# Optimization experiments

Hardware: AMD Instinct MI355X
Metric: run time of the kernel (lower is better)

Reference implementation:

```python
import jax, jax.numpy as jnp
import numpy as np
from jax import lax

B, C_IN, N, K = 4, 128, 4096, 16
C_OUT = 256
EPS = 1e-5


def setup_inputs() -> dict:
    key = jax.random.key(0)
    k1, k2, k3, k4, k5 = jax.random.split(key, 5)
    x = jax.random.normal(k1, (B, C_IN, N, 1), dtype=jnp.float32)
    y = jax.random.normal(k2, (B, C_IN, N, 1), dtype=jnp.float32)
    edge_index = jax.random.randint(k3, (2, B, N, K), 0, N)
    # Conv2d(in=2*C_IN, out=C_OUT, kernel 3x3), kaiming-ish scale
    fan_in = 2 * C_IN * 9
    conv_w = jax.random.normal(k4, (C_OUT, 2 * C_IN, 3, 3), dtype=jnp.float32) * (2.0 / fan_in) ** 0.5
    conv_b = jnp.zeros((C_OUT,), dtype=jnp.float32)
    gamma = jnp.ones((C_OUT,), dtype=jnp.float32)
    beta = jnp.zeros((C_OUT,), dtype=jnp.float32)
    _ = k5
    return {"x": x, "y": y, "edge_index": edge_index,
            "conv_w": conv_w, "conv_b": conv_b, "gamma": gamma, "beta": beta}


def _batched_index_select(feat, idx):
    # feat: [B, C, N, 1], idx: [B, N, K] -> [B, C, N, K]
    fs = feat[..., 0]  # [B, C, N]
    return jax.vmap(lambda fb, ib: fb[:, ib])(fs, idx)


def reference(x, y, edge_index, conv_w, conv_b, gamma, beta):
    x_i = _batched_index_select(x, edge_index[1])        # [B, C, N, K]
    x_j = _batched_index_select(y, edge_index[0])        # [B, C, N, K]
    h = jnp.concatenate([x_i, x_j - x_i], axis=1)        # [B, 2C, N, K]
    out = lax.conv_general_dilated(
        h, conv_w, window_strides=(1, 1), padding=((1, 1), (1, 1)),
        dimension_numbers=("NCHW", "OIHW", "NCHW"))
    out = out + conv_b[None, :, None, None]
    # BatchNorm2d in training mode: biased batch statistics per channel
    mean = jnp.mean(out, axis=(0, 2, 3), keepdims=True)
    var = jnp.mean((out - mean) ** 2, axis=(0, 2, 3), keepdims=True)
    out = gamma[None, :, None, None] * (out - mean) * lax.rsqrt(var + EPS) + beta[None, :, None, None]
    out = jax.nn.relu(out)
    return jnp.max(out, axis=-1, keepdims=True)          # [B, C_OUT, N, 1]
```

## Files before the change

kernel.cpp:

```cpp
#include <hip/hip_runtime.h>

typedef unsigned short u16;
typedef unsigned int u32;
typedef __attribute__((ext_vector_type(8))) u16 u16x8;
typedef __attribute__((ext_vector_type(8))) __bf16 bf16x8;
typedef __attribute__((ext_vector_type(4))) float f32x4;

#define CIN 128
#define NB 4
#define NN 4096
#define KPTS 16
#define COUT 256
#define POSB 65536
#define TOTPOS 262144
#define CK 2304

__device__ __forceinline__ float bf2f(u16 u){ return __uint_as_float(((u32)u)<<16); }
__device__ __forceinline__ u16 f2bf(float f){
  u32 u = __float_as_uint(f);
  u32 r = (u + 0x7fffu + ((u>>16)&1u)) >> 16;
  return (u16)r;
}

__global__ void pack_w_kernel(const float* __restrict__ w, u16* __restrict__ wp){
  int t = blockIdx.x*256 + threadIdx.x;
  if (t >= COUT*CK) return;
  int co = t / CK; int r = t - co*CK; int tap = r >> 8; int c = r & 255;
  float v;
  if (c < 128)
    v = w[(co*256 + c)*9 + tap] - w[(co*256 + 128 + c)*9 + tap];
  else
    v = w[(co*256 + c)*9 + tap];
  wp[t] = f2bf(v);
}

__global__ void transpose_cast_kernel(const float* __restrict__ x, const float* __restrict__ y,
                                      u16* __restrict__ xt, u16* __restrict__ yt){
  __shared__ u16 tile[2][32][65];
  int n0 = blockIdx.x*64, c0 = blockIdx.y*32, b = blockIdx.z;
  int t = threadIdx.x;
  int tn = t & 63, tc = t >> 6;
  #pragma unroll
  for (int i=0;i<8;++i){
    int c = tc*8 + i;
    size_t src = ((size_t)(b*CIN + c0 + c))*NN + n0 + tn;
    tile[0][c][tn] = f2bf(x[src]);
    tile[1][c][tn] = f2bf(y[src]);
  }
  __syncthreads();
  int tcc = t & 31, tnn = t >> 5;
  #pragma unroll
  for (int i=0;i<8;++i){
    int n = tnn*8 + i;
    size_t dst = ((size_t)(b*NN + n0 + n))*CIN + c0 + tcc;
    xt[dst] = tile[0][tcc][n];
    yt[dst] = tile[1][tcc][n];
  }
}

#define SWZ(row, chunk) (((row)*32) + ((((chunk) ^ (((row)>>1)&3))) << 3))

__global__ __launch_bounds__(256) void conv_gemm_kernel(const u16* __restrict__ wp,
    const int* __restrict__ e, const u16* __restrict__ xt, const u16* __restrict__ yt,
    const u16* __restrict__ zrow, const float* __restrict__ bias,
    float* __restrict__ ssum, float* __restrict__ ssq, float* __restrict__ maxout){
  __shared__ u16 als[3*4096];
  __shared__ u16 pnl[2*6144];

  int bid = blockIdx.x;
  int co_half = (bid >> 3) & 1;
  int ptile = (bid & 7) | ((bid >> 4) << 3);
  int p0 = ptile * 128;
  int b = p0 >> 16;
  int pib0 = p0 & (POSB-1);
  int nb0 = pib0 >> 4;

  int t = threadIdx.x;
  int lane = t & 63, wave = t >> 6;
  int wr = wave >> 1, wc = wave & 1;
  int co_base = co_half*128;
  int l15 = lane & 15, l4 = lane >> 4;

  const u16* xb = xt + ((size_t)b)*NN*CIN;
  const u16* yb = yt + ((size_t)b)*NN*CIN;

  int r0 = wave*32 + (lane>>2);
  int r1 = r0 + 16;
  int ch0 = (lane&3) ^ ((r0>>1)&3);
  int ch1 = (lane&3) ^ ((r1>>1)&3);
  int wuni = __builtin_amdgcn_readfirstlane(wave);
  int wu  = wuni*1024;
  int wu2 = wuni*512;
  const u16* pA0 = wp + (size_t)(co_base + r0)*CK + ch0*8;
  const u16* pA1 = wp + (size_t)(co_base + r1)*CK + ch1*8;

  const u16 *xp[3], *yp[3];
  { int tq4 = t >> 2;
    #pragma unroll
    for (int i=0;i<3;++i){
      int row = i*64 + tq4;
      int lc = (t&3) ^ ((row>>1)&3);
      int q = (row*57) >> 10;
      int kk = row - q*18 - 1;
      int n2 = nb0 - 1 + q;
      bool valid = (row < 180) && ((unsigned)n2 < (unsigned)NN) && ((unsigned)kk < (unsigned)KPTS);
      int j0 = 0, j1 = 0;
      if (valid){ int eo = b*POSB + n2*16 + kk; j0 = e[eo]; j1 = e[TOTPOS + eo]; }
      xp[i] = (valid ? xb + (size_t)j1*CIN : zrow) + lc*8;
      yp[i] = (valid ? yb + (size_t)j0*CIN : zrow) + lc*8;
    }
  }

  auto G16 = [&](const u16* g, u16* l){
    __builtin_amdgcn_global_load_lds((const __attribute__((address_space(1))) u32*)g,
                                     (__attribute__((address_space(3))) u32*)l, 16, 0, 0);
  };

  f32x4 acc[4][4];
  #pragma unroll
  for (int i=0;i<4;++i)
    #pragma unroll
    for (int j=0;j<4;++j) acc[i][j] = (f32x4){0.f,0.f,0.f,0.f};

  G16(xp[0],    &pnl[wu2]);
  G16(xp[1],    &pnl[2048+wu2]);
  G16(xp[2],    &pnl[4096+wu2]);
  G16(xp[0]+32, &pnl[6144+wu2]);
  G16(xp[1]+32, &pnl[6144+2048+wu2]);
  G16(xp[2]+32, &pnl[6144+4096+wu2]);
  G16(pA0,      &als[wu]);      G16(pA1,      &als[wu+512]);
  G16(pA0+256,  &als[4096+wu]); G16(pA1+256,  &als[4096+wu+512]);
  G16(pA0+512,  &als[8192+wu]); G16(pA1+512,  &als[8192+wu+512]);

  int aoff[4];
  #pragma unroll
  for (int f=0; f<4; ++f) aoff[f] = SWZ(wr*64 + f*16 + l15, l4);
  int wc72l15 = wc*72 + l15;

  for (int c = 0; c < 8; ++c){
    const u16* pb = pnl + (c&1)*6144;
    int ca = c*32;
    int cc = (c < 7) ? (c+1) : 0;
    const u16 *q0,*q1,*q2;
    if (cc < 4){ q0 = xp[0]+cc*32;     q1 = xp[1]+cc*32;     q2 = xp[2]+cc*32; }
    else       { q0 = yp[0]+(cc-4)*32; q1 = yp[1]+(cc-4)*32; q2 = yp[2]+(cc-4)*32; }
    int pdst = (cc&1)*6144;
    bool doP = (c >= 1) & (c <= 6);
    #pragma unroll
    for (int tap = 0; tap < 9; ++tap){
      asm volatile("s_waitcnt vmcnt(4)" ::: "memory");
      __builtin_amdgcn_s_barrier();
      int abase = (tap%3)*4096;
      bf16x8 af[4], bv[4];
      #pragma unroll
      for (int f=0; f<4; ++f) af[f] = *(bf16x8*)&als[abase + aoff[f]];
      int kbc = (tap/3)*18 + (tap%3);
      #pragma unroll
      for (int f=0; f<4; ++f){
        int r = wc72l15 + kbc + f*18;
        bv[f] = *(bf16x8*)&pb[r*32 + ((l4 ^ ((r>>1)&3))<<3)];
      }
      asm volatile("s_waitcnt lgkmcnt(0)" ::: "memory");
      __builtin_amdgcn_sched_barrier(0);
      __builtin_amdgcn_s_barrier();
      int koff = ((tap+3)%9)*256 + ca + ((tap>5)?32:0);
      G16(pA0 + koff, &als[abase + wu]);
      G16(pA1 + koff, &als[abase + wu + 512]);
      if (tap == 0 && doP){
        G16(q0, &pnl[pdst + wu2]);
        G16(q1, &pnl[pdst + 2048 + wu2]);
        G16(q2, &pnl[pdst + 4096 + wu2]);
      }
      __builtin_amdgcn_s_setprio(1);
      #pragma unroll
      for (int fm=0; fm<4; ++fm)
        #pragma unroll
        for (int fn=0; fn<4; ++fn)
          acc[fm][fn] = __builtin_amdgcn_mfma_f32_16x16x32_bf16(af[fm], bv[fn], acc[fm][fn], 0, 0, 0);
      __builtin_amdgcn_s_setprio(0);
    }
  }
  asm volatile("s_waitcnt vmcnt(0)" ::: "memory");
  __builtin_amdgcn_s_barrier();

  float* fs = (float*)&als[0];
  fs[t & 255] = 0.f;
  __syncthreads();

  #pragma unroll
  for (int fm=0; fm<4; ++fm){
    #pragma unroll
    for (int j=0; j<4; ++j){
      int ch = wr*64 + fm*16 + l4*4 + j;
      int co_g = co_base + ch;
      float bv2 = bias[co_g];
      float s = 0.f, q = 0.f;
      float mv[4];
      #pragma unroll
      for (int fn=0; fn<4; ++fn){
        float v = acc[fm][fn][j] + bv2;
        s += v; q += v*v; mv[fn] = v;
      }
      #pragma unroll
      for (int o=1; o<16; o<<=1){
        s += __shfl_xor(s, o, 64);
        q += __shfl_xor(q, o, 64);
        #pragma unroll
        for (int fn=0; fn<4; ++fn) mv[fn] = fmaxf(mv[fn], __shfl_xor(mv[fn], o, 64));
      }
      if (l15 == 0){
        atomicAdd(&fs[ch], s);
        atomicAdd(&fs[128 + ch], q);
        size_t rowb = ((size_t)(b*COUT + co_g)) << 12;
        #pragma unroll
        for (int fn=0; fn<4; ++fn)
          maxout[rowb + nb0 + wc*4 + fn] = mv[fn];
      }
    }
  }
  __syncthreads();
  if (t < 128)      atomicAdd(&ssum[co_base + t], fs[t]);
  else if (t < 256) atomicAdd(&ssq[co_base + t - 128], fs[t]);
}

__global__ void finalize_stats_kernel(const float* __restrict__ ssum, const float* __restrict__ ssq,
                                      const float* __restrict__ gamma, const float* __restrict__ beta,
                                      float* __restrict__ scale, float* __restrict__ shift){
  int co = threadIdx.x;
  float inv = 1.0f / (float)TOTPOS;
  float mean = ssum[co]*inv;
  float var = ssq[co]*inv - mean*mean;
  float sc = gamma[co] * rsqrtf(var + 1e-5f);
  scale[co] = sc;
  shift[co] = beta[co] - mean*sc;
}

__global__ void bn_finish_kernel(float* __restrict__ out, const float* __restrict__ scale,
                                 const float* __restrict__ shift){
  int t = blockIdx.x*256 + threadIdx.x;
  int co = (t >> 12) & 255;
  float v = out[t];
  out[t] = fmaxf(fmaf(scale[co], v, shift[co]), 0.f);
}

extern "C" void kernel_launch(void* const* d_in, const int* in_sizes, int n_in,
                              void* d_out, int out_size, void* d_ws, size_t ws_size,
                              hipStream_t stream){
  const float* x = (const float*)d_in[0];
  const float* y = (const float*)d_in[1];
  const int*   e = (const int*)d_in[2];
  const float* w = (const float*)d_in[3];
  const float* bias = (const float*)d_in[4];
  const float* gamma = (const float*)d_in[5];
  const float* beta  = (const float*)d_in[6];
  float* out = (float*)d_out;

  char* ws = (char*)d_ws;
  u16*   wp    = (u16*)(ws);
  float* ssum  = (float*)(ws + 1179648);
  float* ssq   = (float*)(ws + 1180672);
  u16*   zrow  = (u16*)(ws + 1181696);
  float* scale = (float*)(ws + 1182720);
  float* shift = (float*)(ws + 1183744);
  u16*   xt    = (u16*)(ws + 1184768);
  u16*   yt    = (u16*)(ws + 5379072);

  hipMemsetAsync(ssum, 0, 3072, stream);

  pack_w_kernel<<<2304, 256, 0, stream>>>(w, wp);
  dim3 tg(NN/64, CIN/32, NB);
  transpose_cast_kernel<<<tg, 256, 0, stream>>>(x, y, xt, yt);
  conv_gemm_kernel<<<4096, 256, 0, stream>>>(wp, e, xt, yt, zrow, bias, ssum, ssq, out);
  finalize_stats_kernel<<<1, COUT, 0, stream>>>(ssum, ssq, gamma, beta, scale, shift);
  bn_finish_kernel<<<out_size/256, 256, 0, stream>>>(out, scale, shift);
}
```

Measured before the change: 350.3 us.

## Double-buffer LDS fragment reads to overlap next-tap loads with MFMA

Restructures the conv main loop into a software pipeline. Fragments for the next tap are read from LDS into a second register set while the MFMAs for the current tap run, and the loop is unrolled across pairs of channel chunks so the register buffers alternate in ping-pong fashion. The goal is to hide LDS read latency and barrier stalls behind matrix compute. The cost is higher register pressure from the second fragment set, which may reduce occupancy. It also requires more intricate vmcnt and barrier ordering, including the panel prefetch wrap-around.

```diff
diff --git a/kernel.cpp b/kernel.cpp
--- a/kernel.cpp
+++ b/kernel.cpp
@@ -137,49 +137,74 @@
   for (int f=0; f<4; ++f) aoff[f] = SWZ(wr*64 + f*16 + l15, l4);
   int wc72l15 = wc*72 + l15;
 
-  for (int c = 0; c < 8; ++c){
-    const u16* pb = pnl + (c&1)*6144;
-    int ca = c*32;
-    int cc = (c < 7) ? (c+1) : 0;
-    const u16 *q0,*q1,*q2;
-    if (cc < 4){ q0 = xp[0]+cc*32;     q1 = xp[1]+cc*32;     q2 = xp[2]+cc*32; }
-    else       { q0 = yp[0]+(cc-4)*32; q1 = yp[1]+(cc-4)*32; q2 = yp[2]+(cc-4)*32; }
-    int pdst = (cc&1)*6144;
-    bool doP = (c >= 1) & (c <= 6);
-    #pragma unroll
-    for (int tap = 0; tap < 9; ++tap){
-      asm volatile("s_waitcnt vmcnt(4)" ::: "memory");
-      __builtin_amdgcn_s_barrier();
-      int abase = (tap%3)*4096;
-      bf16x8 af[4], bv[4];
-      #pragma unroll
-      for (int f=0; f<4; ++f) af[f] = *(bf16x8*)&als[abase + aoff[f]];
-      int kbc = (tap/3)*18 + (tap%3);
-      #pragma unroll
-      for (int f=0; f<4; ++f){
-        int r = wc72l15 + kbc + f*18;
-        bv[f] = *(bf16x8*)&pb[r*32 + ((l4 ^ ((r>>1)&3))<<3)];
-      }
-      asm volatile("s_waitcnt lgkmcnt(0)" ::: "memory");
-      __builtin_amdgcn_sched_barrier(0);
-      __builtin_amdgcn_s_barrier();
-      int koff = ((tap+3)%9)*256 + ca + ((tap>5)?32:0);
-      G16(pA0 + koff, &als[abase + wu]);
-      G16(pA1 + koff, &als[abase + wu + 512]);
-      if (tap == 0 && doP){
-        G16(q0, &pnl[pdst + wu2]);
-        G16(q1, &pnl[pdst + 2048 + wu2]);
-        G16(q2, &pnl[pdst + 4096 + wu2]);
-      }
-      __builtin_amdgcn_s_setprio(1);
-      #pragma unroll
-      for (int fm=0; fm<4; ++fm)
-        #pragma unroll
-        for (int fn=0; fn<4; ++fn)
-          acc[fm][fn] = __builtin_amdgcn_mfma_f32_16x16x32_bf16(af[fm], bv[fn], acc[fm][fn], 0, 0, 0);
-      __builtin_amdgcn_s_setprio(0);
+  bf16x8 f0_a[4], f0_b[4], f1_a[4], f1_b[4];
+
+  asm volatile("s_waitcnt vmcnt(4)" ::: "memory");
+  __builtin_amdgcn_s_barrier();
+  #pragma unroll
+  for (int f=0; f<4; ++f) f0_a[f] = *(bf16x8*)&als[aoff[f]];
+  #pragma unroll
+  for (int f=0; f<4; ++f){
+    int r = wc72l15 + f*18;
+    f0_b[f] = *(bf16x8*)&pnl[r*32 + ((l4 ^ ((r>>1)&3))<<3)];
+  }
+
+  #define STEP(TAU, CUR, NXT) { \
+    asm volatile("s_waitcnt lgkmcnt(0)" ::: "memory"); \
+    __builtin_amdgcn_s_barrier(); \
+    { int chs = (c + (((TAU)>=6)?1:0)) & 7; \
+      int koff = ((((TAU)+3)%9)*256) + (chs<<5); \
+      G16(pA0 + koff, &als[(((TAU)%3)*4096) + wu]); \
+      G16(pA1 + koff, &als[(((TAU)%3)*4096) + wu + 512]); } \
+    if ((TAU)==0){ int cc=(c+1)&7; int co32=(cc&3)*32; \
+      const u16* s0=(cc<4?xp[0]:yp[0])+co32; \
+      const u16* s1=(cc<4?xp[1]:yp[1])+co32; \
+      const u16* s2=(cc<4?xp[2]:yp[2])+co32; \
+      int pd=((c+1)&1)*6144; \
+      G16(s0,&pnl[pd+wu2]); G16(s1,&pnl[pd+2048+wu2]); G16(s2,&pnl[pd+4096+wu2]); } \
+    if ((TAU)<=1) asm volatile("s_waitcnt vmcnt(7)" ::: "memory"); \
+    else          asm volatile("s_waitcnt vmcnt(4)" ::: "memory"); \
+    __builtin_amdgcn_s_barrier(); \
+    if ((c < 7) || ((TAU) < 8)){ \
+      _Pragma("unroll") \
+      for (int f=0; f<4; ++f) NXT##_a[f] = *(bf16x8*)&als[((((TAU)+1)%3)*4096) + aoff[f]]; \
+      const u16* pb = ((TAU)==8) ? pbN : pbC; \
+      const int tq = ((TAU)+1)%9; \
+      const int kbc = (tq/3)*18 + (tq%3); \
+      _Pragma("unroll") \
+      for (int f=0; f<4; ++f){ int r = wc72l15 + kbc + f*18; \
+        NXT##_b[f] = *(bf16x8*)&pb[r*32 + ((l4 ^ ((r>>1)&3))<<3)]; } \
+    } \
+    __builtin_amdgcn_sched_barrier(0); \
+    __builtin_amdgcn_s_setprio(1); \
+    _Pragma("unroll") \
+    for (int fm=0; fm<4; ++fm) \
+      _Pragma("unroll") \
+      for (int fn=0; fn<4; ++fn) \
+        acc[fm][fn] = __builtin_amdgcn_mfma_f32_16x16x32_bf16(CUR##_a[fm], CUR##_b[fn], acc[fm][fn], 0, 0, 0); \
+    __builtin_amdgcn_s_setprio(0); \
+  }
+
+  for (int cp = 0; cp < 8; cp += 2){
+    {
+      int c = cp;
+      const u16* pbC = pnl;
+      const u16* pbN = pnl + 6144;
+      STEP(0, f0, f1)  STEP(1, f1, f0)  STEP(2, f0, f1)
+      STEP(3, f1, f0)  STEP(4, f0, f1)  STEP(5, f1, f0)
+      STEP(6, f0, f1)  STEP(7, f1, f0)  STEP(8, f0, f1)
     }
-  }
+    {
+      int c = cp + 1;
+      const u16* pbC = pnl + 6144;
+      const u16* pbN = pnl;
+      STEP(0, f1, f0)  STEP(1, f0, f1)  STEP(2, f1, f0)
+      STEP(3, f0, f1)  STEP(4, f1, f0)  STEP(5, f0, f1)
+      STEP(6, f1, f0)  STEP(7, f0, f1)  STEP(8, f1, f0)
+    }
+  }
+  #undef STEP
+
   asm volatile("s_waitcnt vmcnt(0)" ::: "memory");
   __builtin_amdgcn_s_barrier();
 
```

Result: slower. 382.2 us (+9.1%).
